# Kernel optimization log

Measured on AMD Instinct MI355X. Metric: run time of the kernel, lower is better.

The kernel has to match this reference:

```python
import jax, jax.numpy as jnp
import numpy as np

NODES = 256
D0, D1 = 0.0, 1.0


def setup_inputs() -> dict:
    key = jax.random.key(0)
    k1, k2 = jax.random.split(key)
    inp = jax.random.uniform(k1, (32, 1024, 1024), dtype=jnp.float32)
    # learnable knot values, initialized as linspace over the domain (as in nn.Parameter)
    value = jnp.linspace(D0, D1, NODES, dtype=jnp.float32)
    # perturb so the spline is non-trivial (still a valid parameter state)
    value = value + 0.1 * jax.random.normal(k2, (NODES,), dtype=jnp.float32)
    return {"input": inp, "value": value}


def _akima_node_slopes(value, h):
    # interval slopes m_i = (v_{i+1}-v_i)/h, shape [n-1]
    m = (value[1:] - value[:-1]) / h
    # Akima boundary extension: two extra slopes on each side
    m_m1 = 2.0 * m[0] - m[1]
    m_m2 = 2.0 * m_m1 - m[0]
    m_p1 = 2.0 * m[-1] - m[-2]
    m_p2 = 2.0 * m_p1 - m[-1]
    me = jnp.concatenate([jnp.stack([m_m2, m_m1]), m, jnp.stack([m_p1, m_p2])])  # [n+3]
    # node derivative s_i = (|m_{i+1}-m_i|*m_{i-1} + |m_{i-1}-m_{i-2}|*m_i) / (sum)
    w1 = jnp.abs(me[3:] - me[2:-1])   # |m_{i+1} - m_i|,      [n]
    w2 = jnp.abs(me[1:-2] - me[:-3])  # |m_{i-1} - m_{i-2}|,  [n]
    mi_1 = me[1:-2]  # m_{i-1}
    mi = me[2:-1]    # m_i
    denom = w1 + w2
    safe = jnp.where(denom > 0, denom, 1.0)
    return jnp.where(denom > 0, (w1 * mi_1 + w2 * mi) / safe, 0.5 * (mi_1 + mi))


def reference(input, value):
    n = value.shape[0]
    h = (D1 - D0) / (n - 1)
    s = _akima_node_slopes(value, h)  # [n]
    x = jnp.clip(input, D0, D1)
    t = (x - D0) / h
    idx = jnp.clip(jnp.floor(t).astype(jnp.int32), 0, n - 2)
    u = t - idx.astype(x.dtype)  # local coordinate in [0,1]
    v0 = value[idx]
    v1 = value[idx + 1]
    s0 = s[idx]
    s1 = s[idx + 1]
    u2 = u * u
    u3 = u2 * u
    h00 = 2.0 * u3 - 3.0 * u2 + 1.0
    h10 = u3 - 2.0 * u2 + u
    h01 = -2.0 * u3 + 3.0 * u2
    h11 = u3 - u2
    return h00 * v0 + h10 * h * s0 + h01 * v1 + h11 * h * s1
```

## Files before the change

kernel.cpp:

```cpp
#include <hip/hip_runtime.h>
#include <hip/hip_bf16.h>

#define NODES 256

__global__ __launch_bounds__(256) void akima_prologue(
    const float* __restrict__ value, float4* __restrict__ tab) {
  __shared__ float me[NODES + 3];
  __shared__ float s[NODES];
  const int t = threadIdx.x;
  const float h = 1.0f / 255.0f;

  if (t < NODES - 1) me[t + 2] = (value[t + 1] - value[t]) / h;
  __syncthreads();

  if (t == 0) {
    float m0 = me[2], m1 = me[3];
    float m_m1 = 2.0f * m0 - m1;
    me[1] = m_m1;
    me[0] = 2.0f * m_m1 - m0;
    float mL = me[NODES];
    float mL1 = me[NODES - 1];
    float m_p1 = 2.0f * mL - mL1;
    me[NODES + 1] = m_p1;
    me[NODES + 2] = 2.0f * m_p1 - mL;
  }
  __syncthreads();

  {
    float w1 = fabsf(me[t + 3] - me[t + 2]);
    float w2 = fabsf(me[t + 1] - me[t]);
    float denom = w1 + w2;
    float sv;
    if (denom > 0.0f)
      sv = (w1 * me[t + 1] + w2 * me[t + 2]) / denom;
    else
      sv = 0.5f * (me[t + 1] + me[t + 2]);
    s[t] = sv;
  }
  __syncthreads();

  if (t < NODES - 1)
    tab[t] = make_float4(value[t], value[t + 1], s[t], s[t + 1]);
}

__global__ __launch_bounds__(256) void akima_main(
    const float* __restrict__ in, const float4* __restrict__ tab,
    float* __restrict__ out, long long n, long long n4) {
  __shared__ float4 stab[NODES - 1];
  if (threadIdx.x < NODES - 1) stab[threadIdx.x] = tab[threadIdx.x];
  __syncthreads();

  const float h = 1.0f / 255.0f;
  const float4* __restrict__ in4 = reinterpret_cast<const float4*>(in);
  float4* __restrict__ out4 = reinterpret_cast<float4*>(out);

  const long long stride = (long long)gridDim.x * blockDim.x;
  long long i0 = (long long)blockIdx.x * blockDim.x + threadIdx.x;

  for (long long i = i0; i < n4; i += stride) {
    float4 x4 = in4[i];
    float xs[4] = {x4.x, x4.y, x4.z, x4.w};
    float r[4];
#pragma unroll
    for (int j = 0; j < 4; ++j) {
      float x = fminf(fmaxf(xs[j], 0.0f), 1.0f);
      float tt = x / h;
      int idx = (int)floorf(tt);
      idx = min(max(idx, 0), NODES - 2);
      float u = tt - (float)idx;
      float4 c = stab[idx];
      float u2 = u * u;
      float u3 = u2 * u;
      float h00 = 2.0f * u3 - 3.0f * u2 + 1.0f;
      float h10 = u3 - 2.0f * u2 + u;
      float h01 = -2.0f * u3 + 3.0f * u2;
      float h11 = u3 - u2;
      r[j] = h00 * c.x + h10 * h * c.z + h01 * c.y + h11 * h * c.w;
    }
    out4[i] = make_float4(r[0], r[1], r[2], r[3]);
  }

  for (long long i = n4 * 4 + i0; i < n; i += stride) {
    float x = fminf(fmaxf(in[i], 0.0f), 1.0f);
    float tt = x / h;
    int idx = (int)floorf(tt);
    idx = min(max(idx, 0), NODES - 2);
    float u = tt - (float)idx;
    float4 c = stab[idx];
    float u2 = u * u;
    float u3 = u2 * u;
    float h00 = 2.0f * u3 - 3.0f * u2 + 1.0f;
    float h10 = u3 - 2.0f * u2 + u;
    float h01 = -2.0f * u3 + 3.0f * u2;
    float h11 = u3 - u2;
    out[i] = h00 * c.x + h10 * h * c.z + h01 * c.y + h11 * h * c.w;
  }
}

extern "C" void kernel_launch(void* const* d_in, const int* in_sizes, int n_in,
                              void* d_out, int out_size, void* d_ws, size_t ws_size,
                              hipStream_t stream) {
  const float* in = (const float*)d_in[0];
  const float* value = (const float*)d_in[1];
  float* out = (float*)d_out;
  float4* tab = (float4*)d_ws;

  long long n = (long long)in_sizes[0];
  long long n4 = n / 4;

  akima_prologue<<<1, 256, 0, stream>>>(value, tab);

  long long want = (n4 + 255) / 256;
  int blocks = (int)(want < 2048 ? (want > 0 ? want : 1) : 2048);
  akima_main<<<blocks, 256, 0, stream>>>(in, tab, out, n, n4);
}
```

Baseline: 233.5 us.

## Split table lookups between LDS and global, add nontemporal streaming loads/stores

Each float4 group now reads the coefficient table for two of its four lanes from LDS and for the other two from the global table (served from L1/L2). The aim is to spread random-gather traffic across LDS and the vector cache so LDS bank conflicts are less of a bottleneck. Input and output now use nontemporal load/store builtins to avoid polluting caches with streaming data. The index math replaces division and floor with a multiply by 255 and integer truncation. That is equivalent for clamped non-negative inputs, but x*255 and x/h can round differently at knot boundaries.

Result: faster. 227.8 us (-2.4%).

```diff
diff --git a/kernel.cpp b/kernel.cpp
--- a/kernel.cpp
+++ b/kernel.cpp
@@ -2,6 +2,8 @@
 #include <hip/hip_bf16.h>
 
 #define NODES 256
+
+typedef float f32x4 __attribute__((ext_vector_type(4)));
 
 __global__ __launch_bounds__(256) void akima_prologue(
     const float* __restrict__ value, float4* __restrict__ tab) {
@@ -12,88 +14,84 @@
 
   if (t < NODES - 1) me[t + 2] = (value[t + 1] - value[t]) / h;
   __syncthreads();
-
   if (t == 0) {
     float m0 = me[2], m1 = me[3];
     float m_m1 = 2.0f * m0 - m1;
     me[1] = m_m1;
     me[0] = 2.0f * m_m1 - m0;
-    float mL = me[NODES];
-    float mL1 = me[NODES - 1];
+    float mL = me[NODES], mL1 = me[NODES - 1];
     float m_p1 = 2.0f * mL - mL1;
     me[NODES + 1] = m_p1;
     me[NODES + 2] = 2.0f * m_p1 - mL;
   }
   __syncthreads();
-
   {
     float w1 = fabsf(me[t + 3] - me[t + 2]);
     float w2 = fabsf(me[t + 1] - me[t]);
     float denom = w1 + w2;
-    float sv;
-    if (denom > 0.0f)
-      sv = (w1 * me[t + 1] + w2 * me[t + 2]) / denom;
-    else
-      sv = 0.5f * (me[t + 1] + me[t + 2]);
-    s[t] = sv;
+    s[t] = (denom > 0.0f) ? (w1 * me[t + 1] + w2 * me[t + 2]) / denom
+                          : 0.5f * (me[t + 1] + me[t + 2]);
   }
   __syncthreads();
-
   if (t < NODES - 1)
     tab[t] = make_float4(value[t], value[t + 1], s[t], s[t + 1]);
 }
 
+__device__ __forceinline__ float akima_eval(float x, const float4& c) {
+  const float h = 1.0f / 255.0f;
+  float tt = fminf(fmaxf(x, 0.0f), 1.0f) * 255.0f;
+  int idx = min(max((int)tt, 0), NODES - 2);
+  float u = tt - (float)idx;
+  float u2 = u * u;
+  float u3 = u2 * u;
+  float h00 = 2.0f * u3 - 3.0f * u2 + 1.0f;
+  float h10 = u3 - 2.0f * u2 + u;
+  float h01 = -2.0f * u3 + 3.0f * u2;
+  float h11 = u3 - u2;
+  return h00 * c.x + h10 * h * c.z + h01 * c.y + h11 * h * c.w;
+}
+
+__device__ __forceinline__ int akima_idx(float x) {
+  float tt = fminf(fmaxf(x, 0.0f), 1.0f) * 255.0f;
+  return min(max((int)tt, 0), NODES - 2);
+}
+
 __global__ __launch_bounds__(256) void akima_main(
-    const float* __restrict__ in, const float4* __restrict__ tab,
+    const float* __restrict__ in, const float4* __restrict__ gtab,
     float* __restrict__ out, long long n, long long n4) {
   __shared__ float4 stab[NODES - 1];
-  if (threadIdx.x < NODES - 1) stab[threadIdx.x] = tab[threadIdx.x];
+  if (threadIdx.x < NODES - 1) stab[threadIdx.x] = gtab[threadIdx.x];
   __syncthreads();
 
-  const float h = 1.0f / 255.0f;
-  const float4* __restrict__ in4 = reinterpret_cast<const float4*>(in);
-  float4* __restrict__ out4 = reinterpret_cast<float4*>(out);
-
+  const f32x4* __restrict__ in4 = reinterpret_cast<const f32x4*>(in);
+  f32x4* __restrict__ out4 = reinterpret_cast<f32x4*>(out);
   const long long stride = (long long)gridDim.x * blockDim.x;
-  long long i0 = (long long)blockIdx.x * blockDim.x + threadIdx.x;
+  const long long i0 = (long long)blockIdx.x * blockDim.x + threadIdx.x;
 
   for (long long i = i0; i < n4; i += stride) {
-    float4 x4 = in4[i];
-    float xs[4] = {x4.x, x4.y, x4.z, x4.w};
-    float r[4];
-#pragma unroll
-    for (int j = 0; j < 4; ++j) {
-      float x = fminf(fmaxf(xs[j], 0.0f), 1.0f);
-      float tt = x / h;
-      int idx = (int)floorf(tt);
-      idx = min(max(idx, 0), NODES - 2);
-      float u = tt - (float)idx;
-      float4 c = stab[idx];
-      float u2 = u * u;
-      float u3 = u2 * u;
-      float h00 = 2.0f * u3 - 3.0f * u2 + 1.0f;
-      float h10 = u3 - 2.0f * u2 + u;
-      float h01 = -2.0f * u3 + 3.0f * u2;
-      float h11 = u3 - u2;
-      r[j] = h00 * c.x + h10 * h * c.z + h01 * c.y + h11 * h * c.w;
-    }
-    out4[i] = make_float4(r[0], r[1], r[2], r[3]);
+    f32x4 x4 = __builtin_nontemporal_load(&in4[i]);
+
+    int ia = akima_idx(x4.x);
+    int ib = akima_idx(x4.y);
+    int ic = akima_idx(x4.z);
+    int id = akima_idx(x4.w);
+    float4 ca = stab[ia];
+    float4 cb = gtab[ib];
+    float4 cc = stab[ic];
+    float4 cd = gtab[id];
+
+    f32x4 r;
+    r.x = akima_eval(x4.x, ca);
+    r.y = akima_eval(x4.y, cb);
+    r.z = akima_eval(x4.z, cc);
+    r.w = akima_eval(x4.w, cd);
+    __builtin_nontemporal_store(r, &out4[i]);
   }
 
   for (long long i = n4 * 4 + i0; i < n; i += stride) {
-    float x = fminf(fmaxf(in[i], 0.0f), 1.0f);
-    float tt = x / h;
-    int idx = (int)floorf(tt);
-    idx = min(max(idx, 0), NODES - 2);
-    float u = tt - (float)idx;
-    float4 c = stab[idx];
-    float u2 = u * u;
-    float u3 = u2 * u;
-    float h00 = 2.0f * u3 - 3.0f * u2 + 1.0f;
-    float h10 = u3 - 2.0f * u2 + u;
-    float h01 = -2.0f * u3 + 3.0f * u2;
-    float h11 = u3 - u2;
-    out[i] = h00 * c.x + h10 * h * c.z + h01 * c.y + h11 * h * c.w;
+    float x = in[i];
+    float4 c = stab[akima_idx(x)];
+    out[i] = akima_eval(x, c);
   }
 }
 
```
